# Performance work log

Measured on AMD Instinct MI355X. Metric: run time of the kernel, lower is better.

The kernel has to match this reference:

```python
import jax, jax.numpy as jnp
import numpy as np

N_NODES = 100000
N_EDGES = 600000
D = 128  # input_dim == output_dim (required by index_add into zeros_like(x) + residual)
EPS = 1e-5


def _linear_params(key, d_in, d_out):
    kw, kb = jax.random.split(key)
    bound = 1.0 / np.sqrt(d_in)
    w = jax.random.uniform(kw, (d_in, d_out), minval=-bound, maxval=bound, dtype=jnp.float32)
    b = jax.random.uniform(kb, (d_out,), minval=-bound, maxval=bound, dtype=jnp.float32)
    return w, b


def setup_inputs() -> dict:
    key = jax.random.key(0)
    ks = jax.random.split(key, 6)
    x = jax.random.normal(ks[0], (N_NODES, D), dtype=jnp.float32)
    edge_index = jax.random.randint(ks[1], (2, N_EDGES), 0, N_NODES, dtype=jnp.int32)
    w_m1, b_m1 = _linear_params(ks[2], 2 * D, D)
    w_m2, b_m2 = _linear_params(ks[3], D, D)
    w_u1, b_u1 = _linear_params(ks[4], 2 * D, D)
    w_u2, b_u2 = _linear_params(ks[5], D, D)
    gamma = jnp.ones((D,), dtype=jnp.float32)
    beta = jnp.zeros((D,), dtype=jnp.float32)
    return {
        "x": x, "edge_index": edge_index,
        "w_m1": w_m1, "b_m1": b_m1, "w_m2": w_m2, "b_m2": b_m2,
        "w_u1": w_u1, "b_u1": b_u1, "w_u2": w_u2, "b_u2": b_u2,
        "gamma": gamma, "beta": beta,
    }


def _layernorm(h, gamma, beta):
    mu = jnp.mean(h, axis=-1, keepdims=True)
    var = jnp.mean(jnp.square(h - mu), axis=-1, keepdims=True)
    return (h - mu) * jax.lax.rsqrt(var + EPS) * gamma + beta


def reference(x, edge_index, w_m1, b_m1, w_m2, b_m2, w_u1, b_u1, w_u2, b_u2, gamma, beta):
    row, col = edge_index[0], edge_index[1]
    # message MLP on concat of gathered endpoints: [E, 2D] -> [E, D]
    m_in = jnp.concatenate([x[row], x[col]], axis=-1)
    m = jax.nn.relu(m_in @ w_m1 + b_m1) @ w_m2 + b_m2
    # scatter-add messages to destination nodes (index_add along dim 0 with col)
    agg = jax.ops.segment_sum(m, col, num_segments=x.shape[0])
    # update MLP on [N, 2D] -> [N, D]
    u_in = jnp.concatenate([x, agg], axis=-1)
    h = jax.nn.relu(u_in @ w_u1 + b_u1) @ w_u2 + b_u2
    return _layernorm(h, gamma, beta) + x
```

## Files before the change

### kernel.cpp

```cpp
#include <hip/hip_runtime.h>
#include <hip/hip_bf16.h>
#include <stdint.h>

#define N_NODES 100000
#define N_EDGES 600000
#define D 128
#define EPS 1e-5f
#define SCAN_BS 512

typedef __attribute__((ext_vector_type(8))) short short8;
typedef __attribute__((ext_vector_type(16))) float floatx16;


__device__ __forceinline__ uint32_t pack_bf16_rne(float lo, float hi) {
    uint32_t ul = __builtin_bit_cast(uint32_t, lo);
    uint32_t uh = __builtin_bit_cast(uint32_t, hi);
    ul += 0x7fffu + ((ul >> 16) & 1u);
    uh += 0x7fffu + ((uh >> 16) & 1u);
    return (ul >> 16) | (uh & 0xffff0000u);
}

__device__ __forceinline__ unsigned short f32_to_bf16_rne(float f) {
    uint32_t u = __builtin_bit_cast(uint32_t, f);
    u += 0x7fffu + ((u >> 16) & 1u);
    return (unsigned short)(u >> 16);
}

__device__ __forceinline__ float bflo(uint32_t a) { return __builtin_bit_cast(float, a << 16); }
__device__ __forceinline__ float bfhi(uint32_t a) { return __builtin_bit_cast(float, a & 0xffff0000u); }


__global__ void hist_kernel(const int* __restrict__ col, int* __restrict__ count) {
    int e = blockIdx.x * blockDim.x + threadIdx.x;
    if (e < N_EDGES) atomicAdd(&count[col[e]], 1);
}

__global__ void scanA_kernel(const int* __restrict__ count, int* __restrict__ base,
                             int* __restrict__ bsum) {
    __shared__ int tmp[SCAN_BS];
    int g = blockIdx.x * SCAN_BS + threadIdx.x;
    int v = (g < N_NODES) ? count[g] : 0;
    tmp[threadIdx.x] = v;
    __syncthreads();
    int acc = v;
#pragma unroll
    for (int off = 1; off < SCAN_BS; off <<= 1) {
        int add = (threadIdx.x >= off) ? tmp[threadIdx.x - off] : 0;
        __syncthreads();
        acc += add;
        tmp[threadIdx.x] = acc;
        __syncthreads();
    }
    if (g < N_NODES) base[g] = acc - v;
    if (threadIdx.x == SCAN_BS - 1) bsum[blockIdx.x] = acc;
}

__global__ void scanB_kernel(int* __restrict__ bsum, int nb) {
    __shared__ int tmp[256];
    int v = (threadIdx.x < nb) ? bsum[threadIdx.x] : 0;
    tmp[threadIdx.x] = v;
    __syncthreads();
    int acc = v;
#pragma unroll
    for (int off = 1; off < 256; off <<= 1) {
        int add = (threadIdx.x >= off) ? tmp[threadIdx.x - off] : 0;
        __syncthreads();
        acc += add;
        tmp[threadIdx.x] = acc;
        __syncthreads();
    }
    if (threadIdx.x < nb) bsum[threadIdx.x] = acc - v;
}

__global__ void scanC_kernel(int* __restrict__ base, const int* __restrict__ bsum,
                             int* __restrict__ cursor) {
    int g = blockIdx.x * SCAN_BS + threadIdx.x;
    if (g < N_NODES) {
        int b = base[g] + bsum[blockIdx.x];
        base[g] = b;
        cursor[g] = b;
    }
}

__global__ void scatter_kernel(const int* __restrict__ row, const int* __restrict__ col,
                               int* __restrict__ cursor, int* __restrict__ srow) {
    int e = blockIdx.x * blockDim.x + threadIdx.x;
    if (e < N_EDGES) {
        int p = atomicAdd(&cursor[col[e]], 1);
        srow[p] = row[e];
    }
}

__global__ void prep_all(const float* __restrict__ w_m1, const float* __restrict__ w_u1,
                         const float* __restrict__ w_u2, const float* __restrict__ w_m2,
                         const float* __restrict__ b_m2,
                         unsigned short* __restrict__ wm1f, unsigned short* __restrict__ wu1tf,
                         unsigned short* __restrict__ wu2f, unsigned short* __restrict__ wcf,
                         float* __restrict__ vb) {
    int idx = blockIdx.x * blockDim.x + threadIdx.x;
    int i = idx, k, n;
    {
        int j    = i & 7;
        int lane = (i >> 3) & 63;
        int t    = (i >> 9) & 3;
        int s    = i >> 11;
        k = (s & 15) * 16 + ((lane >> 5) << 3) + j;
        n = t * 32 + (lane & 31);
    }
    if (idx < 32768) {
        int j = idx & 7, lane = (idx >> 3) & 63, t = (idx >> 9) & 3, s = idx >> 11;
        int kk = s * 16 + ((lane >> 5) << 3) + j;
        wm1f[idx] = f32_to_bf16_rne(w_m1[kk * 128 + t * 32 + (lane & 31)]);
    } else if (idx < 49152) {
        int ii = idx - 32768;
        int j = ii & 7, lane = (ii >> 3) & 63, t = (ii >> 9) & 3, s = ii >> 11;
        int kk = s * 16 + ((lane >> 5) << 3) + j;
        wu1tf[ii] = f32_to_bf16_rne(w_u1[kk * 128 + t * 32 + (lane & 31)]);
    } else if (idx < 65536) {
        int ii = idx - 49152;
        int j = ii & 7, lane = (ii >> 3) & 63, t = (ii >> 9) & 3, s = ii >> 11;
        int kk = s * 16 + ((lane >> 5) << 3) + j;
        wu2f[ii] = f32_to_bf16_rne(w_u2[kk * 128 + t * 32 + (lane & 31)]);
    } else if (idx < 81920) {
        int ii = idx - 65536;
        int j = ii & 7, lane = (ii >> 3) & 63, t = (ii >> 9) & 3, s = ii >> 11;
        int kk = s * 16 + ((lane >> 5) << 3) + j;
        int nn = t * 32 + (lane & 31);
        float acc = 0.0f;
        for (int q = 0; q < 128; ++q)
            acc += w_m2[kk * 128 + q] * w_u1[(128 + q) * 128 + nn];
        wcf[ii] = f32_to_bf16_rne(acc);
    } else if (idx < 82048) {
        int nn = idx - 81920;
        float acc = 0.0f;
        for (int q = 0; q < 128; ++q)
            acc += b_m2[q] * w_u1[(128 + q) * 128 + nn];
        vb[nn] = acc;
    }
}

__launch_bounds__(256, 4)
__global__ void xform_kernel(const float* __restrict__ x, const short8* __restrict__ w1f,
                             const float* __restrict__ b1, unsigned short* __restrict__ xtb) {
    __shared__ __align__(16) short h1[4][32 * 136];
    const int wave = threadIdx.x >> 6;
    const int lane = threadIdx.x & 63;
    const int l31  = lane & 31;
    const int half = lane >> 5;
    short* hl = h1[wave];

    const int nbase = (blockIdx.x * 4 + wave) * 32;
    const int n = min(nbase + l31, N_NODES - 1);
    const float* px = x + (size_t)n * D + half * 8;

    union { short8 v; uint32_t u[4]; } fa[8];
#pragma unroll
    for (int s = 0; s < 8; ++s) {
        const int off = s * 16;
        float4 a0 = *(const float4*)(px + off);
        float4 a1 = *(const float4*)(px + off + 4);
        fa[s].u[0] = pack_bf16_rne(a0.x, a0.y); fa[s].u[1] = pack_bf16_rne(a0.z, a0.w);
        fa[s].u[2] = pack_bf16_rne(a1.x, a1.y); fa[s].u[3] = pack_bf16_rne(a1.z, a1.w);
    }

#pragma unroll
    for (int p = 0; p < 2; ++p) {
        floatx16 acc[4];
#pragma unroll
        for (int t = 0; t < 4; ++t) acc[t] = (floatx16)0.0f;
#pragma unroll
        for (int s = 0; s < 8; ++s) {
#pragma unroll
            for (int t = 0; t < 4; ++t) {
                short8 wf = w1f[((p * 8 + s) * 4 + t) * 64 + lane];
                acc[t] = __builtin_amdgcn_mfma_f32_32x32x16_bf16(fa[s].v, wf, acc[t], 0, 0, 0);
            }
        }
#pragma unroll
        for (int t = 0; t < 4; ++t) {
            float bias = p ? b1[t * 32 + l31] : 0.0f;
#pragma unroll
            for (int r = 0; r < 16; ++r) {
                int m = (r & 3) + 8 * (r >> 2) + 4 * half;
                hl[m * 136 + t * 32 + l31] = (short)f32_to_bf16_rne(acc[t][r] + bias);
            }
        }
#pragma unroll
        for (int it = 0; it < 8; ++it) {
            int off = it * 512 + lane * 8;
            int row = off >> 7;
            int col = off & 127;
            if (nbase + row < N_NODES) {
                short8 v = *(const short8*)(hl + row * 136 + col);
                *(short8*)(xtb + (size_t)(nbase + row) * 256 + p * 128 + col) = v;
            }
        }
    }
}

__launch_bounds__(256, 8)
__global__ void agg_kernel(const uint32_t* __restrict__ xtb32,
                           const int* __restrict__ srow,
                           const int* __restrict__ base, const int* __restrict__ count,
                           uint32_t* __restrict__ hsum) {
    const int node = blockIdx.x * 4 + (threadIdx.x >> 6);
    const int lane = threadIdx.x & 63;
    if (node >= N_NODES) return;

    const int b   = base[node];
    const int deg = count[node];

    const uint32_t xbu = xtb32[(size_t)node * 128 + 64 + lane];
    const float xb_lo = bflo(xbu);
    const float xb_hi = bfhi(xbu);

    float s_lo = 0.0f, s_hi = 0.0f;

    for (int t0 = 0; t0 < deg; t0 += 64) {
        const int nb = min(64, deg - t0);
        int sr = (lane < nb) ? srow[b + t0 + lane] : 0;
        int d = 0;
        for (; d + 4 <= nb; d += 4) {
            int r0 = __shfl(sr, d);
            int r1 = __shfl(sr, d + 1);
            int r2 = __shfl(sr, d + 2);
            int r3 = __shfl(sr, d + 3);
            uint32_t a0 = xtb32[(size_t)r0 * 128 + lane];
            uint32_t a1 = xtb32[(size_t)r1 * 128 + lane];
            uint32_t a2 = xtb32[(size_t)r2 * 128 + lane];
            uint32_t a3 = xtb32[(size_t)r3 * 128 + lane];
            s_lo += fmaxf(bflo(a0) + xb_lo, 0.0f); s_hi += fmaxf(bfhi(a0) + xb_hi, 0.0f);
            s_lo += fmaxf(bflo(a1) + xb_lo, 0.0f); s_hi += fmaxf(bfhi(a1) + xb_hi, 0.0f);
            s_lo += fmaxf(bflo(a2) + xb_lo, 0.0f); s_hi += fmaxf(bfhi(a2) + xb_hi, 0.0f);
            s_lo += fmaxf(bflo(a3) + xb_lo, 0.0f); s_hi += fmaxf(bfhi(a3) + xb_hi, 0.0f);
        }
        if (d + 2 <= nb) {
            int r0 = __shfl(sr, d);
            int r1 = __shfl(sr, d + 1);
            uint32_t a0 = xtb32[(size_t)r0 * 128 + lane];
            uint32_t a1 = xtb32[(size_t)r1 * 128 + lane];
            s_lo += fmaxf(bflo(a0) + xb_lo, 0.0f); s_hi += fmaxf(bfhi(a0) + xb_hi, 0.0f);
            s_lo += fmaxf(bflo(a1) + xb_lo, 0.0f); s_hi += fmaxf(bfhi(a1) + xb_hi, 0.0f);
            d += 2;
        }
        if (d < nb) {
            int r0 = __shfl(sr, d);
            uint32_t a0 = xtb32[(size_t)r0 * 128 + lane];
            s_lo += fmaxf(bflo(a0) + xb_lo, 0.0f); s_hi += fmaxf(bfhi(a0) + xb_hi, 0.0f);
        }
    }
    hsum[(size_t)node * 64 + lane] = pack_bf16_rne(s_lo, s_hi);
}

__launch_bounds__(256, 4)
__global__ void upd_kernel(const float* __restrict__ x, const unsigned short* __restrict__ hsum,
                           const short8* __restrict__ wu1tf, const short8* __restrict__ wcf,
                           const short8* __restrict__ wu2f,
                           const float* __restrict__ b_u1, const float* __restrict__ vb,
                           const int* __restrict__ count,
                           const float* __restrict__ b_u2,
                           const float* __restrict__ gamma, const float* __restrict__ beta,
                           float* __restrict__ out) {
    __shared__ __align__(16) short h1[4][32 * 136];
    const int wave = threadIdx.x >> 6;
    const int lane = threadIdx.x & 63;
    const int l31  = lane & 31;
    const int half = lane >> 5;
    short* hl = h1[wave];

    const int nbase = (blockIdx.x * 4 + wave) * 32;
    const int n = min(nbase + l31, N_NODES - 1);

    const float* px = x + (size_t)n * D + half * 8;
    const unsigned short* ph = hsum + (size_t)n * D + half * 8;

    floatx16 acc[4];
#pragma unroll
    for (int t = 0; t < 4; ++t) acc[t] = (floatx16)0.0f;

#pragma unroll
    for (int s = 0; s < 16; ++s) {
        union { short8 v; uint32_t u[4]; } fa;
        const short8* bf;
        if (s < 8) {
            const int off = s * 16;
            float4 a0 = *(const float4*)(px + off);
            float4 a1 = *(const float4*)(px + off + 4);
            fa.u[0] = pack_bf16_rne(a0.x, a0.y); fa.u[1] = pack_bf16_rne(a0.z, a0.w);
            fa.u[2] = pack_bf16_rne(a1.x, a1.y); fa.u[3] = pack_bf16_rne(a1.z, a1.w);
            bf = wu1tf + (s * 4) * 64;
        } else {
            fa.v = *(const short8*)(ph + (s - 8) * 16);
            bf = wcf + ((s - 8) * 4) * 64;
        }
#pragma unroll
        for (int t = 0; t < 4; ++t) {
            short8 wf = bf[t * 64 + lane];
            acc[t] = __builtin_amdgcn_mfma_f32_32x32x16_bf16(fa.v, wf, acc[t], 0, 0, 0);
        }
    }

    float bu1[4], vbt[4];
#pragma unroll
    for (int t = 0; t < 4; ++t) {
        bu1[t] = b_u1[t * 32 + l31];
        vbt[t] = vb[t * 32 + l31];
    }

#pragma unroll
    for (int r = 0; r < 16; ++r) {
        int m = (r & 3) + 8 * (r >> 2) + 4 * half;
        float dg = (float)count[min(nbase + m, N_NODES - 1)];
#pragma unroll
        for (int t = 0; t < 4; ++t) {
            float v = fmaxf(acc[t][r] + bu1[t] + dg * vbt[t], 0.0f);
            hl[m * 136 + t * 32 + l31] = (short)f32_to_bf16_rne(v);
        }
    }

    floatx16 acc2[4];
#pragma unroll
    for (int t = 0; t < 4; ++t) acc2[t] = (floatx16)0.0f;

#pragma unroll
    for (int s = 0; s < 8; ++s) {
        short8 af = *(const short8*)(hl + l31 * 136 + s * 16 + half * 8);
#pragma unroll
        for (int t = 0; t < 4; ++t) {
            short8 wf = wu2f[(s * 4 + t) * 64 + lane];
            acc2[t] = __builtin_amdgcn_mfma_f32_32x32x16_bf16(af, wf, acc2[t], 0, 0, 0);
        }
    }

    float g4[4], be4[4], bias2[4];
#pragma unroll
    for (int t = 0; t < 4; ++t) {
        g4[t]    = gamma[t * 32 + l31];
        be4[t]   = beta[t * 32 + l31];
        bias2[t] = b_u2[t * 32 + l31];
    }

#pragma unroll
    for (int r = 0; r < 16; ++r) {
        float hv[4];
        float s1 = 0.0f, s2 = 0.0f;
#pragma unroll
        for (int t = 0; t < 4; ++t) {
            hv[t] = acc2[t][r] + bias2[t];
            s1 += hv[t];
            s2 += hv[t] * hv[t];
        }
#pragma unroll
        for (int mask = 1; mask < 32; mask <<= 1) {
            s1 += __shfl_xor(s1, mask);
            s2 += __shfl_xor(s2, mask);
        }
        float mean = s1 * (1.0f / 128.0f);
        float var  = s2 * (1.0f / 128.0f) - mean * mean;
        float rs   = rsqrtf(var + EPS);
        int m = (r & 3) + 8 * (r >> 2) + 4 * half;
        int node = nbase + m;
        if (node < N_NODES) {
            const float* xr = x + (size_t)node * D + l31;
            float* orow = out + (size_t)node * D + l31;
#pragma unroll
            for (int t = 0; t < 4; ++t) {
                float v = (hv[t] - mean) * rs * g4[t] + be4[t] + xr[t * 32];
                orow[t * 32] = v;
            }
        }
    }
}

extern "C" void kernel_launch(void* const* d_in, const int* in_sizes, int n_in,
                              void* d_out, int out_size, void* d_ws, size_t ws_size,
                              hipStream_t stream) {
    const float* x     = (const float*)d_in[0];
    const int*   edge  = (const int*)d_in[1];
    const float* w_m1  = (const float*)d_in[2];
    const float* b_m1  = (const float*)d_in[3];
    const float* w_m2  = (const float*)d_in[4];
    const float* b_m2  = (const float*)d_in[5];
    const float* w_u1  = (const float*)d_in[6];
    const float* b_u1  = (const float*)d_in[7];
    const float* w_u2  = (const float*)d_in[8];
    const float* b_u2  = (const float*)d_in[9];
    const float* gamma = (const float*)d_in[10];
    const float* beta  = (const float*)d_in[11];
    float* out = (float*)d_out;

    char* ws = (char*)d_ws;
    size_t off = 0;
    auto alloc = [&](size_t bytes) { void* p = ws + off; off = (off + bytes + 15) & ~(size_t)15; return p; };

    unsigned short* xtb   = (unsigned short*)alloc((size_t)N_NODES * 256 * 2);
    unsigned short* hsumB = (unsigned short*)alloc((size_t)N_NODES * D * 2);
    unsigned short* wm1f  = (unsigned short*)alloc(256 * 128 * 2);
    unsigned short* wu1tf = (unsigned short*)alloc(128 * 128 * 2);
    unsigned short* wcf   = (unsigned short*)alloc(128 * 128 * 2);
    unsigned short* wu2f  = (unsigned short*)alloc(128 * 128 * 2);
    float* vb    = (float*)alloc(128 * 4);
    int* count   = (int*)alloc((size_t)N_NODES * 4);
    int* base    = (int*)alloc((size_t)N_NODES * 4);
    int* cursor  = (int*)alloc((size_t)N_NODES * 4);
    int* bsum    = (int*)alloc(256 * 4);
    int* srow    = (int*)alloc((size_t)N_EDGES * 4);

    const int* rowi = edge;
    const int* coli = edge + N_EDGES;
    const int NB = (N_NODES + SCAN_BS - 1) / SCAN_BS;

    (void)hipMemsetAsync(count, 0, (size_t)N_NODES * 4, stream);

    prep_all<<<(82048 + 255) / 256, 256, 0, stream>>>(
        w_m1, w_u1, w_u2, w_m2, b_m2, wm1f, wu1tf, wu2f, wcf, vb);

    hist_kernel<<<(N_EDGES + 255) / 256, 256, 0, stream>>>(coli, count);
    scanA_kernel<<<NB, SCAN_BS, 0, stream>>>(count, base, bsum);
    scanB_kernel<<<1, 256, 0, stream>>>(bsum, NB);
    scanC_kernel<<<NB, SCAN_BS, 0, stream>>>(base, bsum, cursor);
    scatter_kernel<<<(N_EDGES + 255) / 256, 256, 0, stream>>>(rowi, coli, cursor, srow);

    xform_kernel<<<(N_NODES + 127) / 128, 256, 0, stream>>>(
        x, (const short8*)wm1f, b_m1, xtb);
    agg_kernel<<<(N_NODES + 3) / 4, 256, 0, stream>>>(
        (const uint32_t*)xtb, srow, base, count, (uint32_t*)hsumB);
    upd_kernel<<<(N_NODES + 127) / 128, 256, 0, stream>>>(
        x, hsumB, (const short8*)wu1tf, (const short8*)wcf, (const short8*)wu2f,
        b_u1, vb, count, b_u2, gamma, beta, out);
}
```

Before: 291.7 us.

## Merge preprocessing kernels, single-pass scan, and coalesce update epilogue through LDS

The weight-prep and histogram kernels are merged into one launch, and the scatter is merged into the xform kernel by extra blocks. The three-kernel scan becomes one pass that gets block offsets from an atomic counter. Because those offsets follow block arrival order rather than block index, the CSR layout may not be node-ordered, but each node's range still holds all of its edges. The update kernel preloads its hsum fragments, fetches degrees with one load plus shuffles, and stages layernorm output in LDS so the residual add and store use coalesced float4 accesses. The aim is to cut launch count and make the final stores efficient.

```diff
diff --git a/kernel.cpp b/kernel.cpp
--- a/kernel.cpp
+++ b/kernel.cpp
@@ -7,6 +7,10 @@
 #define D 128
 #define EPS 1e-5f
 #define SCAN_BS 512
+
+#define PREP_BLOCKS 321
+#define HIST_BLOCKS 2344
+#define XF_BLOCKS   782
 
 typedef __attribute__((ext_vector_type(8))) short short8;
 typedef __attribute__((ext_vector_type(16))) float floatx16;
@@ -29,84 +33,19 @@
 __device__ __forceinline__ float bflo(uint32_t a) { return __builtin_bit_cast(float, a << 16); }
 __device__ __forceinline__ float bfhi(uint32_t a) { return __builtin_bit_cast(float, a & 0xffff0000u); }
 
-
-__global__ void hist_kernel(const int* __restrict__ col, int* __restrict__ count) {
-    int e = blockIdx.x * blockDim.x + threadIdx.x;
-    if (e < N_EDGES) atomicAdd(&count[col[e]], 1);
-}
-
-__global__ void scanA_kernel(const int* __restrict__ count, int* __restrict__ base,
-                             int* __restrict__ bsum) {
-    __shared__ int tmp[SCAN_BS];
-    int g = blockIdx.x * SCAN_BS + threadIdx.x;
-    int v = (g < N_NODES) ? count[g] : 0;
-    tmp[threadIdx.x] = v;
-    __syncthreads();
-    int acc = v;
-#pragma unroll
-    for (int off = 1; off < SCAN_BS; off <<= 1) {
-        int add = (threadIdx.x >= off) ? tmp[threadIdx.x - off] : 0;
-        __syncthreads();
-        acc += add;
-        tmp[threadIdx.x] = acc;
-        __syncthreads();
-    }
-    if (g < N_NODES) base[g] = acc - v;
-    if (threadIdx.x == SCAN_BS - 1) bsum[blockIdx.x] = acc;
-}
-
-__global__ void scanB_kernel(int* __restrict__ bsum, int nb) {
-    __shared__ int tmp[256];
-    int v = (threadIdx.x < nb) ? bsum[threadIdx.x] : 0;
-    tmp[threadIdx.x] = v;
-    __syncthreads();
-    int acc = v;
-#pragma unroll
-    for (int off = 1; off < 256; off <<= 1) {
-        int add = (threadIdx.x >= off) ? tmp[threadIdx.x - off] : 0;
-        __syncthreads();
-        acc += add;
-        tmp[threadIdx.x] = acc;
-        __syncthreads();
-    }
-    if (threadIdx.x < nb) bsum[threadIdx.x] = acc - v;
-}
-
-__global__ void scanC_kernel(int* __restrict__ base, const int* __restrict__ bsum,
-                             int* __restrict__ cursor) {
-    int g = blockIdx.x * SCAN_BS + threadIdx.x;
-    if (g < N_NODES) {
-        int b = base[g] + bsum[blockIdx.x];
-        base[g] = b;
-        cursor[g] = b;
-    }
-}
-
-__global__ void scatter_kernel(const int* __restrict__ row, const int* __restrict__ col,
-                               int* __restrict__ cursor, int* __restrict__ srow) {
-    int e = blockIdx.x * blockDim.x + threadIdx.x;
-    if (e < N_EDGES) {
-        int p = atomicAdd(&cursor[col[e]], 1);
-        srow[p] = row[e];
-    }
-}
-
-__global__ void prep_all(const float* __restrict__ w_m1, const float* __restrict__ w_u1,
-                         const float* __restrict__ w_u2, const float* __restrict__ w_m2,
-                         const float* __restrict__ b_m2,
-                         unsigned short* __restrict__ wm1f, unsigned short* __restrict__ wu1tf,
-                         unsigned short* __restrict__ wu2f, unsigned short* __restrict__ wcf,
-                         float* __restrict__ vb) {
-    int idx = blockIdx.x * blockDim.x + threadIdx.x;
-    int i = idx, k, n;
-    {
-        int j    = i & 7;
-        int lane = (i >> 3) & 63;
-        int t    = (i >> 9) & 3;
-        int s    = i >> 11;
-        k = (s & 15) * 16 + ((lane >> 5) << 3) + j;
-        n = t * 32 + (lane & 31);
-    }
+__global__ void prep_hist(const float* __restrict__ w_m1, const float* __restrict__ w_u1,
+                          const float* __restrict__ w_u2, const float* __restrict__ w_m2,
+                          const float* __restrict__ b_m2,
+                          unsigned short* __restrict__ wm1f, unsigned short* __restrict__ wu1tf,
+                          unsigned short* __restrict__ wu2f, unsigned short* __restrict__ wcf,
+                          float* __restrict__ vb,
+                          const int* __restrict__ col, int* __restrict__ count) {
+    if (blockIdx.x >= PREP_BLOCKS) {
+        int e = (blockIdx.x - PREP_BLOCKS) * 256 + threadIdx.x;
+        if (e < N_EDGES) atomicAdd(&count[col[e]], 1);
+        return;
+    }
+    int idx = blockIdx.x * 256 + threadIdx.x;
     if (idx < 32768) {
         int j = idx & 7, lane = (idx >> 3) & 63, t = (idx >> 9) & 3, s = idx >> 11;
         int kk = s * 16 + ((lane >> 5) << 3) + j;
@@ -139,9 +78,46 @@
     }
 }
 
+__global__ void scan_one(const int* __restrict__ count, int* __restrict__ base,
+                         int* __restrict__ cursor, int* __restrict__ gcur) {
+    __shared__ int tmp[SCAN_BS];
+    __shared__ int bbase;
+    int g = blockIdx.x * SCAN_BS + threadIdx.x;
+    int v = (g < N_NODES) ? count[g] : 0;
+    tmp[threadIdx.x] = v;
+    __syncthreads();
+    int acc = v;
+#pragma unroll
+    for (int off = 1; off < SCAN_BS; off <<= 1) {
+        int add = (threadIdx.x >= off) ? tmp[threadIdx.x - off] : 0;
+        __syncthreads();
+        acc += add;
+        tmp[threadIdx.x] = acc;
+        __syncthreads();
+    }
+    if (threadIdx.x == SCAN_BS - 1) bbase = atomicAdd(gcur, acc);
+    __syncthreads();
+    if (g < N_NODES) {
+        int b = bbase + acc - v;
+        base[g] = b;
+        cursor[g] = b;
+    }
+}
+
 __launch_bounds__(256, 4)
-__global__ void xform_kernel(const float* __restrict__ x, const short8* __restrict__ w1f,
-                             const float* __restrict__ b1, unsigned short* __restrict__ xtb) {
+__global__ void xform_scatter(const float* __restrict__ x, const short8* __restrict__ w1f,
+                              const float* __restrict__ b1, unsigned short* __restrict__ xtb,
+                              const int* __restrict__ row, const int* __restrict__ col,
+                              int* __restrict__ cursor, int* __restrict__ srow) {
+    if (blockIdx.x >= XF_BLOCKS) {
+        int e = (blockIdx.x - XF_BLOCKS) * 256 + threadIdx.x;
+        if (e < N_EDGES) {
+            int p = atomicAdd(&cursor[col[e]], 1);
+            srow[p] = row[e];
+        }
+        return;
+    }
+
     __shared__ __align__(16) short h1[4][32 * 136];
     const int wave = threadIdx.x >> 6;
     const int lane = threadIdx.x & 63;
@@ -188,11 +164,11 @@
 #pragma unroll
         for (int it = 0; it < 8; ++it) {
             int off = it * 512 + lane * 8;
-            int row = off >> 7;
-            int col = off & 127;
-            if (nbase + row < N_NODES) {
-                short8 v = *(const short8*)(hl + row * 136 + col);
-                *(short8*)(xtb + (size_t)(nbase + row) * 256 + p * 128 + col) = v;
+            int r2 = off >> 7;
+            int c2 = off & 127;
+            if (nbase + r2 < N_NODES) {
+                short8 v = *(const short8*)(hl + r2 * 136 + c2);
+                *(short8*)(xtb + (size_t)(nbase + r2) * 256 + p * 128 + c2) = v;
             }
         }
     }
@@ -274,6 +250,12 @@
     const float* px = x + (size_t)n * D + half * 8;
     const unsigned short* ph = hsum + (size_t)n * D + half * 8;
 
+    short8 hfr[8];
+#pragma unroll
+    for (int s = 0; s < 8; ++s) hfr[s] = *(const short8*)(ph + s * 16);
+
+    float dgv = (float)count[min(nbase + l31, N_NODES - 1)];
+
     floatx16 acc[4];
 #pragma unroll
     for (int t = 0; t < 4; ++t) acc[t] = (floatx16)0.0f;
@@ -290,7 +272,7 @@
             fa.u[2] = pack_bf16_rne(a1.x, a1.y); fa.u[3] = pack_bf16_rne(a1.z, a1.w);
             bf = wu1tf + (s * 4) * 64;
         } else {
-            fa.v = *(const short8*)(ph + (s - 8) * 16);
+            fa.v = hfr[s - 8];
             bf = wcf + ((s - 8) * 4) * 64;
         }
 #pragma unroll
@@ -310,7 +292,7 @@
 #pragma unroll
     for (int r = 0; r < 16; ++r) {
         int m = (r & 3) + 8 * (r >> 2) + 4 * half;
-        float dg = (float)count[min(nbase + m, N_NODES - 1)];
+        float dg = __shfl(dgv, m, 32);
 #pragma unroll
         for (int t = 0; t < 4; ++t) {
             float v = fmaxf(acc[t][r] + bu1[t] + dg * vbt[t], 0.0f);
@@ -340,33 +322,45 @@
         bias2[t] = b_u2[t * 32 + l31];
     }
 
-#pragma unroll
-    for (int r = 0; r < 16; ++r) {
-        float hv[4];
-        float s1 = 0.0f, s2 = 0.0f;
-#pragma unroll
-        for (int t = 0; t < 4; ++t) {
-            hv[t] = acc2[t][r] + bias2[t];
-            s1 += hv[t];
-            s2 += hv[t] * hv[t];
-        }
-#pragma unroll
-        for (int mask = 1; mask < 32; mask <<= 1) {
-            s1 += __shfl_xor(s1, mask);
-            s2 += __shfl_xor(s2, mask);
-        }
-        float mean = s1 * (1.0f / 128.0f);
-        float var  = s2 * (1.0f / 128.0f) - mean * mean;
-        float rs   = rsqrtf(var + EPS);
-        int m = (r & 3) + 8 * (r >> 2) + 4 * half;
-        int node = nbase + m;
-        if (node < N_NODES) {
-            const float* xr = x + (size_t)node * D + l31;
-            float* orow = out + (size_t)node * D + l31;
+    float* hf = (float*)hl;
+#pragma unroll
+    for (int p = 0; p < 2; ++p) {
+#pragma unroll
+        for (int rr = 0; rr < 8; ++rr) {
+            int r = p * 8 + rr;
+            float hv[4];
+            float s1 = 0.0f, s2 = 0.0f;
 #pragma unroll
             for (int t = 0; t < 4; ++t) {
-                float v = (hv[t] - mean) * rs * g4[t] + be4[t] + xr[t * 32];
-                orow[t * 32] = v;
+                hv[t] = acc2[t][r] + bias2[t];
+                s1 += hv[t];
+                s2 += hv[t] * hv[t];
+            }
+#pragma unroll
+            for (int mask = 1; mask < 32; mask <<= 1) {
+                s1 += __shfl_xor(s1, mask);
+                s2 += __shfl_xor(s2, mask);
+            }
+            float mean = s1 * (1.0f / 128.0f);
+            float var  = s2 * (1.0f / 128.0f) - mean * mean;
+            float rs   = rsqrtf(var + EPS);
+            int m = (r & 3) + 8 * (r >> 2) + 4 * half;
+            int mrow = m - 16 * p;
+#pragma unroll
+            for (int t = 0; t < 4; ++t)
+                hf[mrow * 132 + t * 32 + l31] = (hv[t] - mean) * rs * g4[t] + be4[t];
+        }
+#pragma unroll
+        for (int it = 0; it < 8; ++it) {
+            int q = it * 64 + lane;
+            int r2 = q >> 5;
+            int c4 = q & 31;
+            int node = nbase + 16 * p + r2;
+            if (node < N_NODES) {
+                float4 v = *(const float4*)(hf + r2 * 132 + c4 * 4);
+                float4 xr = *(const float4*)(x + (size_t)node * D + c4 * 4);
+                v.x += xr.x; v.y += xr.y; v.z += xr.z; v.w += xr.w;
+                *(float4*)(out + (size_t)node * D + c4 * 4) = v;
             }
         }
     }
@@ -400,29 +394,26 @@
     unsigned short* wcf   = (unsigned short*)alloc(128 * 128 * 2);
     unsigned short* wu2f  = (unsigned short*)alloc(128 * 128 * 2);
     float* vb    = (float*)alloc(128 * 4);
-    int* count   = (int*)alloc((size_t)N_NODES * 4);
+    int* count   = (int*)alloc((size_t)N_NODES * 4 + 16);
+    int* gcur    = count + N_NODES;
     int* base    = (int*)alloc((size_t)N_NODES * 4);
     int* cursor  = (int*)alloc((size_t)N_NODES * 4);
-    int* bsum    = (int*)alloc(256 * 4);
     int* srow    = (int*)alloc((size_t)N_EDGES * 4);
 
     const int* rowi = edge;
     const int* coli = edge + N_EDGES;
     const int NB = (N_NODES + SCAN_BS - 1) / SCAN_BS;
 
-    (void)hipMemsetAsync(count, 0, (size_t)N_NODES * 4, stream);
-
-    prep_all<<<(82048 + 255) / 256, 256, 0, stream>>>(
-        w_m1, w_u1, w_u2, w_m2, b_m2, wm1f, wu1tf, wu2f, wcf, vb);
-
-    hist_kernel<<<(N_EDGES + 255) / 256, 256, 0, stream>>>(coli, count);
-    scanA_kernel<<<NB, SCAN_BS, 0, stream>>>(count, base, bsum);
-    scanB_kernel<<<1, 256, 0, stream>>>(bsum, NB);
-    scanC_kernel<<<NB, SCAN_BS, 0, stream>>>(base, bsum, cursor);
-    scatter_kernel<<<(N_EDGES + 255) / 256, 256, 0, stream>>>(rowi, coli, cursor, srow);
-
-    xform_kernel<<<(N_NODES + 127) / 128, 256, 0, stream>>>(
-        x, (const short8*)wm1f, b_m1, xtb);
+    (void)hipMemsetAsync(count, 0, (size_t)N_NODES * 4 + 16, stream);
+
+    prep_hist<<<PREP_BLOCKS + HIST_BLOCKS, 256, 0, stream>>>(
+        w_m1, w_u1, w_u2, w_m2, b_m2, wm1f, wu1tf, wu2f, wcf, vb, coli, count);
+
+    scan_one<<<NB, SCAN_BS, 0, stream>>>(count, base, cursor, gcur);
+
+    xform_scatter<<<XF_BLOCKS + HIST_BLOCKS, 256, 0, stream>>>(
+        x, (const short8*)wm1f, b_m1, xtb, rowi, coli, cursor, srow);
+
     agg_kernel<<<(N_NODES + 3) / 4, 256, 0, stream>>>(
         (const uint32_t*)xtb, srow, base, count, (uint32_t*)hsumB);
     upd_kernel<<<(N_NODES + 127) / 128, 256, 0, stream>>>(
```

Measured after the change: 271.1 us. 7.1% less time.
